# Optimization experiments

Hardware: AMD Instinct MI355X
Metric: run time of the kernel (lower is better)

Reference implementation:

```python
import jax, jax.numpy as jnp
import numpy as np

B, T, C, H = 2, 2048, 1024, 16
D = C // H  # 64
RW, RA, RG = 64, 64, 128  # decay / a / gate LoRA ranks
EPS = 1e-5


def setup_inputs() -> dict:
    key = jax.random.key(0)
    ks = iter(jax.random.split(key, 40))
    n = lambda s, sc=0.02: jax.random.normal(next(ks), s, jnp.float32) * sc
    u = lambda s: jax.random.uniform(next(ks), s, jnp.float32)
    return dict(
        hidden_states=jax.random.normal(next(ks), (B, T, C), jnp.float32),
        # token-mix (time-shift lerp) params
        x_r=u((C,)), x_w=u((C,)), x_k=u((C,)), x_v=u((C,)), x_a=u((C,)), x_g=u((C,)),
        k_k=u((C,)), k_a=u((C,)), r_k=n((H, D), 0.1),
        # square projections (stored [in, out]; x @ W)
        W_r=n((C, C)), W_k=n((C, C)), W_v=n((C, C)), W_o=n((C, C)),
        # LoRA: out = act(x @ A) @ Bm + bias (activation between the two linears)
        w_lora_a=n((C, RW)), w_lora_b=n((RW, C)), w_lora_bias=n((C,), 0.1),
        a_lora_a=n((C, RA)), a_lora_b=n((RA, C)), a_lora_bias=jnp.zeros((C,), jnp.float32),
        g_lora_a=n((C, RG)), g_lora_b=n((RG, C)), g_lora_bias=jnp.zeros((C,), jnp.float32),
        # GroupNorm(num_heads groups over value_dim)
        gn_weight=jnp.ones((C,), jnp.float32), gn_bias=jnp.zeros((C,), jnp.float32),
    )


def _rwkv7_scan(r, log_w, k, v, a, b):
    # all inputs [B, T, H, D]; state S: [B, H, D_v, D_k]
    # S_t = S_{t-1} * diag(exp(log_w_t)) + (S_{t-1} @ a_t) b_t^T + v_t k_t^T
    # o_t = S_t @ r_t
    Bn, Tn, Hn, Dn = r.shape

    def step(S, xs):
        r_t, w_t, k_t, v_t, a_t, b_t = xs  # each [B, H, D]
        sa = jnp.einsum('bhij,bhj->bhi', S, a_t)          # S @ a (pre-decay state)
        S = (S * jnp.exp(w_t)[:, :, None, :]
             + sa[..., None] * b_t[:, :, None, :]
             + v_t[..., None] * k_t[:, :, None, :])
        o_t = jnp.einsum('bhij,bhj->bhi', S, r_t)
        return S, o_t

    S0 = jnp.zeros((Bn, Hn, Dn, Dn), r.dtype)
    xs = tuple(jnp.swapaxes(x, 0, 1) for x in (r, log_w, k, v, a, b))  # [T,B,H,D]
    _, o = jax.lax.scan(step, S0, xs)
    return jnp.swapaxes(o, 0, 1)  # [B, T, H, D]


def reference(hidden_states, x_r, x_w, x_k, x_v, x_a, x_g, k_k, k_a, r_k,
              W_r, W_k, W_v, W_o,
              w_lora_a, w_lora_b, w_lora_bias,
              a_lora_a, a_lora_b, a_lora_bias,
              g_lora_a, g_lora_b, g_lora_bias,
              gn_weight, gn_bias):
    Bn, Tn, Cn = hidden_states.shape
    # time shift: pad one step of zeros at the front, drop last
    shifted = jnp.concatenate([jnp.zeros_like(hidden_states[:, :1]), hidden_states[:, :-1]], axis=1)
    delta = shifted - hidden_states

    xr = hidden_states + delta * x_r
    xw = hidden_states + delta * x_w
    xk = hidden_states + delta * x_k
    xv = hidden_states + delta * x_v
    xa = hidden_states + delta * x_a

    r = xr @ W_r
    log_w = -jax.nn.softplus(-((jnp.tanh(xw @ w_lora_a) @ w_lora_b) + w_lora_bias)) - 0.5
    k = xk @ W_k
    v = xv @ W_v
    a = jax.nn.sigmoid((xa @ a_lora_a) @ a_lora_b + a_lora_bias)
    # g_lora(r): sigmoid activation sits BETWEEN the two LoRA linears
    g = jax.nn.sigmoid(r @ g_lora_a) @ g_lora_b + g_lora_bias

    kk = (k * k_k).reshape(Bn, Tn, H, D)
    kk = kk / jnp.maximum(jnp.linalg.norm(kk, axis=-1, keepdims=True), 1e-12)  # per-head L2 norm
    k = k * (1.0 + (a - 1.0) * k_a)

    rh = r.reshape(Bn, Tn, H, D)
    wh = log_w.reshape(Bn, Tn, H, D)
    kh = k.reshape(Bn, Tn, H, D)
    vh = v.reshape(Bn, Tn, H, D)
    ah = a.reshape(Bn, Tn, H, D)

    o = _rwkv7_scan(rh, wh, kh, vh, -kk, kk * ah)  # [B, T, H, D]

    # GroupNorm over value_dim with H groups (stats per head)
    mu = o.mean(-1, keepdims=True)
    var = ((o - mu) ** 2).mean(-1, keepdims=True)
    o_flat = ((o - mu) * jax.lax.rsqrt(var + EPS)).reshape(Bn, Tn, C) * gn_weight + gn_bias

    bonus = ((rh * kh * r_k).sum(-1, keepdims=True) * vh).reshape(Bn, Tn, C)
    o_flat = o_flat + bonus
    return (o_flat * g) @ W_o
```

## Files before the change

### kernel.cpp

```cpp
#include <hip/hip_runtime.h>
#include <hip/hip_bf16.h>
#include <hip/hip_fp16.h>
#include <stdint.h>
#include <stddef.h>

typedef __hip_bfloat16 bf16;
typedef _Float16 f16;
typedef __attribute__((ext_vector_type(8))) short short8;
typedef __attribute__((ext_vector_type(8))) _Float16 half8;
typedef __attribute__((ext_vector_type(4))) float f32x4;
typedef __attribute__((ext_vector_type(2))) float f32x2;
typedef unsigned short us;

__device__ __forceinline__ float dsigm(float z){ return 1.f/(1.f+expf(-z)); }

template<int CTRL>
__device__ __forceinline__ float dpp_term(float x) {
  int xi = __builtin_bit_cast(int, x);
  int yi = __builtin_amdgcn_update_dpp(0, xi, CTRL, 0xF, 0xF, false);
  return __builtin_bit_cast(float, yi);
}
__device__ __forceinline__ float red8(float x) {
  x += dpp_term<0xB1>(x);
  x += dpp_term<0x4E>(x);
  x += dpp_term<0x141>(x);
  return x;
}

__device__ __forceinline__ void split1(float v, us& h, us& l) {
  bf16 hb = __float2bfloat16(v);
  h = __builtin_bit_cast(us, hb);
  float hf = __bfloat162float(hb);
  bf16 lb = __float2bfloat16(v - hf);
  l = __builtin_bit_cast(us, lb);
}

__device__ __forceinline__ void split8(const float* f, short8& h, short8& l) {
#pragma unroll
  for (int e = 0; e < 8; ++e) {
    us hh, ll;
    split1(f[e], hh, ll);
    h[e] = (short)hh; l[e] = (short)ll;
  }
}

__device__ __forceinline__ void gl16(const f16* g, f16* l) {
  __builtin_amdgcn_global_load_lds((const __attribute__((address_space(1))) void*)g,
                                   (__attribute__((address_space(3))) void*)l, 16, 0, 0);
}

__device__ __forceinline__ void emit16(const float* __restrict__ marr, int c4,
    const float4& cur, const float4& dlt, f16* __restrict__ out, int row)
{
  float4 m = *(const float4*)(marr + c4);
  f16* o = out + (size_t)row*1024 + c4;
  o[0] = (f16)fmaf(dlt.x, m.x, cur.x);
  o[1] = (f16)fmaf(dlt.y, m.y, cur.y);
  o[2] = (f16)fmaf(dlt.z, m.z, cur.z);
  o[3] = (f16)fmaf(dlt.w, m.w, cur.w);
}

__global__ void k_prep(const float* __restrict__ hs,
    const float* __restrict__ mr, const float* __restrict__ mw, const float* __restrict__ mk,
    const float* __restrict__ mv, const float* __restrict__ ma,
    f16* __restrict__ oxr, f16* __restrict__ oxw, f16* __restrict__ oxk,
    f16* __restrict__ oxv, f16* __restrict__ oxa)
{
  int id = blockIdx.x * 256 + threadIdx.x;
  int row = id >> 8;
  int c4 = (id & 255) << 2;
  int t = row & 2047;
  const float* hp = hs + (size_t)row*1024 + c4;
  float4 cur = *(const float4*)hp;
  float4 prev = make_float4(0.f,0.f,0.f,0.f);
  if (t > 0) prev = *(const float4*)(hp - 1024);
  float4 dlt = make_float4(prev.x-cur.x, prev.y-cur.y, prev.z-cur.z, prev.w-cur.w);
  emit16(mr, c4, cur, dlt, oxr, row);
  emit16(mw, c4, cur, dlt, oxw, row);
  emit16(mk, c4, cur, dlt, oxk, row);
  emit16(mv, c4, cur, dlt, oxv, row);
  emit16(ma, c4, cur, dlt, oxa, row);
}

struct SrcP { const float* p[10]; };
struct DstP { f16* p[10]; };

__global__ void k_transpose(SrcP S, DstP Dd)
{
  static constexpr int TR[10]  = {1024,1024,1024,1024,1024,  64,1024,  64,1024, 128};
  static constexpr int TCC[10] = {1024,1024,1024,1024,  64,1024,  64,1024, 128,1024};
  static constexpr int TCP[10] = {1024,1024,1024,1024, 128,1024, 128,1024, 128,1024};
  int z = blockIdx.z;
  int R = TR[z], Cc = TCC[z], Cp = TCP[z];
  int n0 = blockIdx.x * 32, r0 = blockIdx.y * 32;
  if (n0 >= Cp || r0 >= R) return;
  const float* src = S.p[z];
  f16* dst = Dd.p[z];
  int tx = threadIdx.x, ty = threadIdx.y;
  __shared__ float tile[32][33];
  if (n0 < Cc) {
#pragma unroll
    for (int i = 0; i < 4; ++i)
      tile[ty + 8*i][tx] = src[(size_t)(r0 + ty + 8*i)*Cc + n0 + tx];
    __syncthreads();
#pragma unroll
    for (int i = 0; i < 4; ++i)
      dst[(size_t)(n0 + ty + 8*i)*R + r0 + tx] = (f16)tile[tx][ty + 8*i];
  } else {
#pragma unroll
    for (int i = 0; i < 4; ++i)
      dst[(size_t)(n0 + ty + 8*i)*R + r0 + tx] = (f16)0.f;
  }
}

struct GJob {
  const f16* A;
  const f16* Bt;
  float* C;
  f16* Cpk;
  const float* bias;
  int K; int N; int Npk; int ldc; int act;
  int lda; int ldb;
};
struct GJobs { GJob j[5]; };

__global__ __launch_bounds__(256) void k_gemm_fp16(GJobs jobs)
{
  GJob jb = jobs.j[blockIdx.z];
  const int colBase = blockIdx.y * 128;
  if (colBase >= jb.N) return;
  const int rowBase = blockIdx.x * 128;
  __shared__ __align__(16) f16 As[128*32];
  __shared__ __align__(16) f16 Bs[128*32];
  const int tid = threadIdx.x;
  const int l = tid & 63, w = tid >> 6;
  const int wm = w >> 1, wn = w & 1;
  const int lrow = l & 15, kid = (l >> 4) * 8;
  const int nk = jb.K >> 5;

  const int s0 = w*64 + l, s1 = (4 + w)*64 + l;
  const int ar0 = s0 >> 2, ac0 = (s0 & 3) * 8;
  const int ar1 = s1 >> 2, ac1 = (s1 & 3) * 8;
  const int ld0 = w*512, ld1 = (4 + w)*512;
  const f16* Arow0 = jb.A  + (size_t)(rowBase + ar0)*jb.lda + ac0;
  const f16* Arow1 = jb.A  + (size_t)(rowBase + ar1)*jb.lda + ac1;
  const f16* Brow0 = jb.Bt + (size_t)(colBase + ar0)*jb.ldb + ac0;
  const f16* Brow1 = jb.Bt + (size_t)(colBase + ar1)*jb.ldb + ac1;

  f32x4 acc[4][4];
#pragma unroll
  for (int i = 0; i < 4; ++i)
#pragma unroll
    for (int j = 0; j < 4; ++j) { f32x4 z = {0.f,0.f,0.f,0.f}; acc[i][j] = z; }

  for (int kt = 0; kt < nk; ++kt) {
    const int kh = kt*32;
    gl16(Arow0 + kh, &As[ld0]);  gl16(Arow1 + kh, &As[ld1]);
    gl16(Brow0 + kh, &Bs[ld0]);  gl16(Brow1 + kh, &Bs[ld1]);
    __syncthreads();
    half8 ah[4], bh[4];
#pragma unroll
    for (int mt = 0; mt < 4; ++mt) ah[mt] = *(const half8*)&As[(wm*64 + mt*16 + lrow)*32 + kid];
#pragma unroll
    for (int nt = 0; nt < 4; ++nt) bh[nt] = *(const half8*)&Bs[(wn*64 + nt*16 + lrow)*32 + kid];
#pragma unroll
    for (int mt = 0; mt < 4; ++mt)
#pragma unroll
      for (int nt = 0; nt < 4; ++nt)
        acc[mt][nt] = __builtin_amdgcn_mfma_f32_16x16x32_f16(ah[mt], bh[nt], acc[mt][nt], 0, 0, 0);
    __syncthreads();
  }
#pragma unroll
  for (int mt = 0; mt < 4; ++mt) {
    int row = rowBase + wm*64 + mt*16 + (l >> 4)*4;
#pragma unroll
    for (int nt = 0; nt < 4; ++nt) {
      int col = colBase + wn*64 + nt*16 + (l & 15);
      float bv = (jb.bias != nullptr) ? jb.bias[col] : 0.f;
#pragma unroll
      for (int rg = 0; rg < 4; ++rg) {
        float v = acc[mt][nt][rg] + bv;
        if (jb.act == 1)      v = dsigm(v);
        else if (jb.act == 2) v = tanhf(v);
        else if (jb.act == 3) v = 0.60653066f * dsigm(v);
        if (jb.C) jb.C[(size_t)(row + rg)*jb.ldc + col] = v;
        if (jb.Cpk && col < jb.Npk)
          jb.Cpk[(size_t)(row + rg)*jb.Npk + col] = (f16)v;
      }
    }
  }
}

__global__ void k_scanprep(f16* __restrict__ kA, f16* __restrict__ aA,
                           const float* __restrict__ kkw, const float* __restrict__ kaw,
                           f16* __restrict__ kkA)
{
  int idx = blockIdx.x * 256 + threadIdx.x;
  size_t gt8 = (size_t)idx * 8;
  int ch = (int)(gt8 & 1023);
  half8 k8 = *(const half8*)(kA + gt8);
  half8 a8 = *(const half8*)(aA + gt8);
  float kw[8], ka_[8];
  *(float4*)&kw[0]  = *(const float4*)(kkw + ch);
  *(float4*)&kw[4]  = *(const float4*)(kkw + ch + 4);
  *(float4*)&ka_[0] = *(const float4*)(kaw + ch);
  *(float4*)&ka_[4] = *(const float4*)(kaw + ch + 4);
  float kkv[8]; float ss = 0.f;
#pragma unroll
  for (int e = 0; e < 8; ++e) { kkv[e] = (float)k8[e] * kw[e]; ss += kkv[e]*kkv[e]; }
  ss += __shfl_xor(ss, 1); ss += __shfl_xor(ss, 2); ss += __shfl_xor(ss, 4);
  float inv = 1.f / fmaxf(sqrtf(ss), 1e-12f);
  half8 kkn8, bb8, kup8;
#pragma unroll
  for (int e = 0; e < 8; ++e) {
    float kkn = kkv[e] * inv;
    float av = (float)a8[e];
    kkn8[e] = (f16)kkn;
    bb8[e]  = (f16)(kkn * av);
    kup8[e] = (f16)((float)k8[e] * fmaf(av - 1.f, ka_[e], 1.f));
  }
  *(half8*)(kkA + gt8) = kkn8;
  *(half8*)(aA + gt8)  = bb8;
  *(half8*)(kA + gt8)  = kup8;
}

__device__ __forceinline__ void step_pk(const float* __restrict__ sb, int s,
    f32x2* u2, f32x2* p2, float* __restrict__ o0A, float* __restrict__ zA,
    size_t base, int i, int q, int j0)
{
  f32x2 ew2[4], kk2[4], bb2[4], kv2[4], rr2[4];
#pragma unroll
  for (int hh = 0; hh < 2; ++hh) {
    float4 a0 = *(const float4*)(sb + 0    + s*64 + j0 + hh*4);
    float4 a1 = *(const float4*)(sb + 512  + s*64 + j0 + hh*4);
    float4 a2 = *(const float4*)(sb + 1024 + s*64 + j0 + hh*4);
    float4 a3 = *(const float4*)(sb + 1536 + s*64 + j0 + hh*4);
    float4 a4 = *(const float4*)(sb + 2048 + s*64 + j0 + hh*4);
    ew2[hh*2+0] = f32x2{a0.x, a0.y}; ew2[hh*2+1] = f32x2{a0.z, a0.w};
    kk2[hh*2+0] = f32x2{a1.x, a1.y}; kk2[hh*2+1] = f32x2{a1.z, a1.w};
    bb2[hh*2+0] = f32x2{a2.x, a2.y}; bb2[hh*2+1] = f32x2{a2.z, a2.w};
    kv2[hh*2+0] = f32x2{a3.x, a3.y}; kv2[hh*2+1] = f32x2{a3.z, a3.w};
    rr2[hh*2+0] = f32x2{a4.x, a4.y}; rr2[hh*2+1] = f32x2{a4.z, a4.w};
  }
  float vi = sb[2560 + s*64 + i];

  f32x2 uk2 = u2[0]*kk2[0], pk2 = p2[0]*kk2[0];
#pragma unroll
  for (int e = 1; e < 4; ++e) { uk2 += u2[e]*kk2[e]; pk2 += p2[e]*kk2[e]; }
  float uk = red8(uk2.x + uk2.y);
  float pk = red8(pk2.x + pk2.y);
  const f32x2 su2 = {-uk, -uk}, sp2 = {-pk, -pk}, vi2 = {vi, vi};
  f32x2 oo2 = {0.f, 0.f}, zz2 = {0.f, 0.f};
#pragma unroll
  for (int e = 0; e < 4; ++e) {
    f32x2 uu = u2[e]*ew2[e] + su2*bb2[e] + vi2*kv2[e];
    u2[e] = uu; oo2 += uu*rr2[e];
    f32x2 pp = p2[e]*ew2[e] + sp2*bb2[e];
    p2[e] = pp; zz2 += pp*rr2[e];
  }
  float oo = red8(oo2.x + oo2.y);
  float zz = red8(zz2.x + zz2.y);
  if (q == 0) { o0A[base + i] = oo; zA[base + i] = zz; }
}

__global__ __launch_bounds__(512) void k_scan_p1(
    const f16* __restrict__ rA, const f16* __restrict__ ewA,
    const f16* __restrict__ kA, const f16* __restrict__ vA,
    const f16* __restrict__ kkA, const f16* __restrict__ bbA,
    float* __restrict__ o0A, float* __restrict__ zA,
    float* __restrict__ UcA, float* __restrict__ PTcA)
{
  const int blk = blockIdx.x;
  const int bh = blk & 31, c = blk >> 5;
  const int b = bh >> 4, h = bh & 15;
  const int tid = threadIdx.x;
  const int i = tid >> 3, q = tid & 7, j0 = q * 8;
  const size_t base0 = (size_t)b*2048*1024 + (size_t)h*64 + (size_t)(c*64)*1024;

  __shared__ __align__(16) float smem[6144];

  const int active = (tid < 384);
  const int a0 = tid >> 6, rm0 = tid & 63, s0 = rm0 >> 3, f0 = rm0 & 7;
  const f16* pa0 = (a0==0) ? ewA : (a0==1) ? kkA : (a0==2) ? bbA :
                   (a0==3) ? kA  : (a0==4) ? rA  : vA;
  const f16* src0 = pa0 + base0 + (size_t)s0*1024 + f0*8;
  const int dst0 = a0*512 + s0*64 + f0*8;

  f32x2 u2[4], p2[4];
#pragma unroll
  for (int e = 0; e < 4; ++e) {
    u2[e] = f32x2{0.f, 0.f};
    float p0 = (j0 + 2*e     == i) ? 1.f : 0.f;
    float p1 = (j0 + 2*e + 1 == i) ? 1.f : 0.f;
    p2[e] = f32x2{p0, p1};
  }

  if (active) {
    half8 hh = *(const half8*)(src0);
    float4 lo = {(float)hh[0], (float)hh[1], (float)hh[2], (float)hh[3]};
    float4 hi = {(float)hh[4], (float)hh[5], (float)hh[6], (float)hh[7]};
    *(float4*)&smem[dst0]     = lo;
    *(float4*)&smem[dst0 + 4] = hi;
  }
  __syncthreads();

  int curb = 0;
  for (int g = 0; g < 8; ++g) {
    half8 n0;
    if (g < 7 && active) n0 = *(const half8*)(src0 + (size_t)(g+1)*8192);
    const float* sb = smem + curb*3072;
#pragma unroll
    for (int s = 0; s < 8; ++s)
      step_pk(sb, s, u2, p2, o0A, zA, base0 + (size_t)(g*8 + s)*1024, i, q, j0);
    if (g < 7 && active) {
      float4 lo = {(float)n0[0], (float)n0[1], (float)n0[2], (float)n0[3]};
      float4 hi = {(float)n0[4], (float)n0[5], (float)n0[6], (float)n0[7]};
      *(float4*)&smem[(curb^1)*3072 + dst0]     = lo;
      *(float4*)&smem[(curb^1)*3072 + dst0 + 4] = hi;
    }
    __syncthreads();
    curb ^= 1;
  }

  const size_t cbase = ((size_t)(bh*32 + c)) * 4096;
  *(float4*)(UcA + cbase + (size_t)i*64 + j0)     = make_float4(u2[0].x,u2[0].y,u2[1].x,u2[1].y);
  *(float4*)(UcA + cbase + (size_t)i*64 + j0 + 4) = make_float4(u2[2].x,u2[2].y,u2[3].x,u2[3].y);
  float (*lds)[65] = (float(*)[65])smem;
#pragma unroll
  for (int e = 0; e < 4; ++e) {
    lds[i][j0 + 2*e]     = p2[e].x;
    lds[i][j0 + 2*e + 1] = p2[e].y;
  }
  __syncthreads();
  float4 w0 = make_float4(lds[j0+0][i], lds[j0+1][i], lds[j0+2][i], lds[j0+3][i]);
  float4 w1 = make_float4(lds[j0+4][i], lds[j0+5][i], lds[j0+6][i], lds[j0+7][i]);
  *(float4*)(PTcA + cbase + (size_t)i*64 + j0)     = w0;
  *(float4*)(PTcA + cbase + (size_t)i*64 + j0 + 4) = w1;
}

__device__ __forceinline__ void chain_body(int c, int bh, int w, int lr, int lq,
    float (&Slds)[64][65], f32x4 (&acc)[4],
    float (&u_c)[4][4], float4 (&p_c)[2][2],
    float (&u_n)[4][4], float4 (&p_n)[2][2],
    const float* __restrict__ UcA, const float* __restrict__ PTcA,
    float* __restrict__ S0A)
{
  const size_t s0base = ((size_t)bh*32 + c) * 4096;
#pragma unroll
  for (int mt = 0; mt < 4; ++mt)
#pragma unroll
    for (int rg = 0; rg < 4; ++rg) {
      Slds[mt*16 + lq*4 + rg][w*16 + lr] = acc[mt][rg];
      if (c > 0) S0A[s0base + (size_t)(mt*16 + lq*4 + rg)*64 + w*16 + lr] = acc[mt][rg];
    }
  __syncthreads();
  if (c + 1 < 32) {
    const size_t nbase = ((size_t)bh*32 + c + 1) * 4096;
#pragma unroll
    for (int mt = 0; mt < 4; ++mt)
#pragma unroll
      for (int rg = 0; rg < 4; ++rg)
        u_n[mt][rg] = UcA[nbase + (size_t)(mt*16 + lq*4 + rg)*64 + w*16 + lr];
#pragma unroll
    for (int kt = 0; kt < 2; ++kt)
#pragma unroll
      for (int hh = 0; hh < 2; ++hh)
        p_n[kt][hh] = *(const float4*)(PTcA + nbase + (size_t)(w*16 + lr)*64 + kt*32 + lq*8 + hh*4);
  }
  short8 pbh[2], pbl[2];
#pragma unroll
  for (int kt = 0; kt < 2; ++kt) {
    float f[8] = {p_c[kt][0].x, p_c[kt][0].y, p_c[kt][0].z, p_c[kt][0].w,
                  p_c[kt][1].x, p_c[kt][1].y, p_c[kt][1].z, p_c[kt][1].w};
    split8(f, pbh[kt], pbl[kt]);
  }
  f32x4 nacc[4];
#pragma unroll
  for (int mt = 0; mt < 4; ++mt) {
    f32x4 z = {u_c[mt][0], u_c[mt][1], u_c[mt][2], u_c[mt][3]};
    nacc[mt] = z;
  }
#pragma unroll
  for (int kt = 0; kt < 2; ++kt)
#pragma unroll
    for (int mt = 0; mt < 4; ++mt) {
      float f[8];
#pragma unroll
      for (int e = 0; e < 8; ++e) f[e] = Slds[mt*16 + lr][kt*32 + lq*8 + e];
      short8 sah, sal;
      split8(f, sah, sal);
      nacc[mt] = __builtin_amdgcn_mfma_f32_16x16x32_bf16(sah, pbh[kt], nacc[mt], 0, 0, 0);
      nacc[mt] = __builtin_amdgcn_mfma_f32_16x16x32_bf16(sal, pbh[kt], nacc[mt], 0, 0, 0);
      nacc[mt] = __builtin_amdgcn_mfma_f32_16x16x32_bf16(sah, pbl[kt], nacc[mt], 0, 0, 0);
    }
#pragma unroll
  for (int mt = 0; mt < 4; ++mt) acc[mt] = nacc[mt];
  __syncthreads();
}

__global__ __launch_bounds__(256) void k_chain(
    const float* __restrict__ UcA, const float* __restrict__ PTcA,
    float* __restrict__ S0A)
{
  const int bh = blockIdx.x;
  const int l = threadIdx.x & 63, w = threadIdx.x >> 6;
  const int lr = l & 15, lq = l >> 4;
  __shared__ float Slds[64][65];

  f32x4 acc[4];
#pragma unroll
  for (int mt = 0; mt < 4; ++mt) { f32x4 z = {0.f,0.f,0.f,0.f}; acc[mt] = z; }

  float u0[4][4], u1[4][4];
  float4 p0[2][2], p1[2][2];
  {
    const size_t cbase = (size_t)bh * 32 * 4096;
#pragma unroll
    for (int mt = 0; mt < 4; ++mt)
#pragma unroll
      for (int rg = 0; rg < 4; ++rg)
        u0[mt][rg] = UcA[cbase + (size_t)(mt*16 + lq*4 + rg)*64 + w*16 + lr];
#pragma unroll
    for (int kt = 0; kt < 2; ++kt)
#pragma unroll
      for (int hh = 0; hh < 2; ++hh)
        p0[kt][hh] = *(const float4*)(PTcA + cbase + (size_t)(w*16 + lr)*64 + kt*32 + lq*8 + hh*4);
  }
  for (int c = 0; c < 32; c += 2) {
    chain_body(c,     bh, w, lr, lq, Slds, acc, u0, p0, u1, p1, UcA, PTcA, S0A);
    chain_body(c + 1, bh, w, lr, lq, Slds, acc, u1, p1, u0, p0, UcA, PTcA, S0A);
  }
}

__global__ __launch_bounds__(256) void k_corrpost(
    const float* __restrict__ S0A, const float* __restrict__ zA,
    const float* __restrict__ o0A, const f16* __restrict__ rA,
    const f16* __restrict__ kA, const f16* __restrict__ vA,
    const float* __restrict__ rk, const float* __restrict__ gnw,
    const float* __restrict__ gnb, const f16* __restrict__ gA,
    f16* __restrict__ yH)
{
  const int blk = blockIdx.x;
  const int bh = blk & 31;
  const int c  = blk >> 5;
  const int b = bh >> 4, h = bh & 15;
  const int l = threadIdx.x & 63, w = threadIdx.x >> 6;
  const int lr = l & 15, lq = l >> 4;

  f32x4 a2[4];
#pragma unroll
  for (int nt = 0; nt < 4; ++nt) { f32x4 z = {0.f,0.f,0.f,0.f}; a2[nt] = z; }

  if (c > 0) {
    const size_t s0base = ((size_t)bh*32 + c) * 4096;
    short8 sbh[4][2], sbl[4][2];
#pragma unroll
    for (int nt = 0; nt < 4; ++nt)
#pragma unroll
      for (int kt = 0; kt < 2; ++kt) {
        float f[8];
#pragma unroll
        for (int e = 0; e < 8; ++e)
          f[e] = S0A[s0base + (size_t)(nt*16 + lr)*64 + kt*32 + lq*8 + e];
        split8(f, sbh[nt][kt], sbl[nt][kt]);
      }
    short8 zh[2], zl[2];
#pragma unroll
    for (int kt = 0; kt < 2; ++kt) {
      const float* zp = zA + ((size_t)(b*2048 + c*64 + w*16 + lr)*16 + h)*64 + kt*32 + lq*8;
      float f[8];
#pragma unroll
      for (int e = 0; e < 8; ++e) f[e] = zp[e];
      split8(f, zh[kt], zl[kt]);
    }
#pragma unroll
    for (int kt = 0; kt < 2; ++kt)
#pragma unroll
      for (int nt = 0; nt < 4; ++nt) {
        a2[nt] = __builtin_amdgcn_mfma_f32_16x16x32_bf16(zh[kt], sbh[nt][kt], a2[nt], 0, 0, 0);
        a2[nt] = __builtin_amdgcn_mfma_f32_16x16x32_bf16(zl[kt], sbh[nt][kt], a2[nt], 0, 0, 0);
        a2[nt] = __builtin_amdgcn_mfma_f32_16x16x32_bf16(zh[kt], sbl[nt][kt], a2[nt], 0, 0, 0);
      }
  }

#pragma unroll
  for (int rg = 0; rg < 4; ++rg) {
    const int tl = w*16 + lq*4 + rg;
    const size_t trow = (size_t)(b*2048 + c*64 + tl);
    const size_t rb = trow*1024 + h*64;
    float o4[4], v4[4];
    float sum = 0.f, pr = 0.f;
#pragma unroll
    for (int nt = 0; nt < 4; ++nt) {
      const int ii = nt*16 + lr;
      float o = o0A[rb + ii] + a2[nt][rg];
      o4[nt] = o; sum += o;
      v4[nt] = (float)vA[rb + ii];
      pr += (float)rA[rb + ii] * (float)kA[rb + ii] * rk[h*64 + ii];
    }
    sum += __shfl_xor(sum,1); sum += __shfl_xor(sum,2);
    sum += __shfl_xor(sum,4); sum += __shfl_xor(sum,8);
    pr  += __shfl_xor(pr,1);  pr  += __shfl_xor(pr,2);
    pr  += __shfl_xor(pr,4);  pr  += __shfl_xor(pr,8);
    float mean = sum * (1.f/64.f);
    float vp = 0.f;
#pragma unroll
    for (int nt = 0; nt < 4; ++nt) { float d = o4[nt]-mean; vp += d*d; }
    vp += __shfl_xor(vp,1); vp += __shfl_xor(vp,2);
    vp += __shfl_xor(vp,4); vp += __shfl_xor(vp,8);
    float inv = rsqrtf(vp*(1.f/64.f) + 1e-5f);
#pragma unroll
    for (int nt = 0; nt < 4; ++nt) {
      const int ii = nt*16 + lr;
      const int ch = h*64 + ii;
      float y = (o4[nt]-mean)*inv*gnw[ch] + gnb[ch];
      y = fmaf(pr, v4[nt], y);
      y *= (float)gA[rb + ii];
      yH[trow*1024 + ch] = (f16)y;
    }
  }
}

extern "C" void kernel_launch(void* const* d_in, const int* in_sizes, int n_in,
                              void* d_out, int out_size, void* d_ws, size_t ws_size,
                              hipStream_t stream)
{
  (void)in_sizes; (void)n_in; (void)out_size; (void)ws_size;
  const float* hs     = (const float*)d_in[0];
  const float* x_r    = (const float*)d_in[1];
  const float* x_w    = (const float*)d_in[2];
  const float* x_k    = (const float*)d_in[3];
  const float* x_v    = (const float*)d_in[4];
  const float* x_a    = (const float*)d_in[5];
  const float* k_k    = (const float*)d_in[7];
  const float* k_a    = (const float*)d_in[8];
  const float* r_k    = (const float*)d_in[9];
  const float* W_r    = (const float*)d_in[10];
  const float* W_k    = (const float*)d_in[11];
  const float* W_v    = (const float*)d_in[12];
  const float* W_o    = (const float*)d_in[13];
  const float* wla    = (const float*)d_in[14];
  const float* wlb    = (const float*)d_in[15];
  const float* wlbias = (const float*)d_in[16];
  const float* ala    = (const float*)d_in[17];
  const float* alb    = (const float*)d_in[18];
  const float* albias = (const float*)d_in[19];
  const float* gla    = (const float*)d_in[20];
  const float* glb    = (const float*)d_in[21];
  const float* glbias = (const float*)d_in[22];
  const float* gnw    = (const float*)d_in[23];
  const float* gnb    = (const float*)d_in[24];

  char* ws = (char*)d_ws;
  size_t cur = 0;
  auto take = [&](size_t bytes) { size_t o = cur; cur += (bytes + 255) & ~(size_t)255; return o; };

  f16* xr_h = (f16*)(ws + take((size_t)4096*1024*2));
  f16* xw_h = (f16*)(ws + take((size_t)4096*1024*2));
  f16* xk_h = (f16*)(ws + take((size_t)4096*1024*2));
  f16* xv_h = (f16*)(ws + take((size_t)4096*1024*2));
  f16* xa_h = (f16*)(ws + take((size_t)4096*1024*2));
  f16* Wr_p  = (f16*)(ws + take((size_t)1024*1024*2));
  f16* Wk_p  = (f16*)(ws + take((size_t)1024*1024*2));
  f16* Wv_p  = (f16*)(ws + take((size_t)1024*1024*2));
  f16* Wo_p  = (f16*)(ws + take((size_t)1024*1024*2));
  f16* wla_p = (f16*)(ws + take((size_t)128*1024*2));
  f16* wlb_p = (f16*)(ws + take((size_t)1024*64*2));
  f16* ala_p = (f16*)(ws + take((size_t)128*1024*2));
  f16* alb_p = (f16*)(ws + take((size_t)1024*64*2));
  f16* gla_p = (f16*)(ws + take((size_t)128*1024*2));
  f16* glb_p = (f16*)(ws + take((size_t)1024*128*2));
  f16* r_h  = (f16*)(ws + take((size_t)4096*1024*2));
  f16* k_h  = (f16*)(ws + take((size_t)4096*1024*2));
  f16* v_h  = (f16*)(ws + take((size_t)4096*1024*2));
  f16* kk_h = (f16*)(ws + take((size_t)4096*1024*2));
  f16* g_h  = (f16*)(ws + take((size_t)4096*1024*2));
  f16* t2w  = (f16*)(ws + take((size_t)4096*64*2));
  f16* t2a  = (f16*)(ws + take((size_t)4096*64*2));
  f16* t2g  = (f16*)(ws + take((size_t)4096*128*2));
  float* z_f  = (float*)(ws + take((size_t)4096*1024*4));
  float* Uc_f = (float*)(ws + take((size_t)4096*1024*4));
  float* PT_f = (float*)(ws + take((size_t)4096*1024*4));
  f16*   ew_h = xw_h;
  f16*   a_h  = xa_h;
  f16*   y_h  = xr_h;
  float* S0_f = (float*)xk_h;
  float* oF   = (float*)d_out;

  k_prep<<<4096, 256, 0, stream>>>(hs, x_r, x_w, x_k, x_v, x_a,
                                   xr_h, xw_h, xk_h, xv_h, xa_h);
  SrcP sp; DstP dp;
  sp.p[0]=W_r; sp.p[1]=W_k; sp.p[2]=W_v; sp.p[3]=W_o;
  sp.p[4]=wla; sp.p[5]=wlb; sp.p[6]=ala; sp.p[7]=alb; sp.p[8]=gla; sp.p[9]=glb;
  dp.p[0]=Wr_p; dp.p[1]=Wk_p; dp.p[2]=Wv_p; dp.p[3]=Wo_p;
  dp.p[4]=wla_p; dp.p[5]=wlb_p; dp.p[6]=ala_p; dp.p[7]=alb_p; dp.p[8]=gla_p; dp.p[9]=glb_p;
  k_transpose<<<dim3(32,32,10), dim3(32,8), 0, stream>>>(sp, dp);

  GJobs J{};
  auto job = [](const f16* A, const f16* Bt, float* C, f16* Cpk, const float* bias,
                int K, int N, int Npk, int ldc, int act, int lda, int ldb) {
    GJob j; j.A=A; j.Bt=Bt; j.C=C; j.Cpk=Cpk; j.bias=bias;
    j.K=K; j.N=N; j.Npk=Npk; j.ldc=ldc; j.act=act; j.lda=lda; j.ldb=ldb;
    return j;
  };

  J.j[0] = job(xr_h, Wr_p,  nullptr, r_h, nullptr, 1024, 1024, 1024, 0, 0, 1024, 1024);
  J.j[1] = job(xk_h, Wk_p,  nullptr, k_h, nullptr, 1024, 1024, 1024, 0, 0, 1024, 1024);
  J.j[2] = job(xv_h, Wv_p,  nullptr, v_h, nullptr, 1024, 1024, 1024, 0, 0, 1024, 1024);
  J.j[3] = job(xw_h, wla_p, nullptr, t2w, nullptr, 1024, 128,  64,   0, 2, 1024, 1024);
  J.j[4] = job(xa_h, ala_p, nullptr, t2a, nullptr, 1024, 128,  64,   0, 0, 1024, 1024);
  k_gemm_fp16<<<dim3(32,8,5), 256, 0, stream>>>(J);

  J = GJobs{};
  J.j[0] = job(t2w, wlb_p, nullptr, ew_h, wlbias, 64,   1024, 1024, 0, 3, 64,   64);
  J.j[1] = job(t2a, alb_p, nullptr, a_h,  albias, 64,   1024, 1024, 0, 1, 64,   64);
  J.j[2] = job(r_h, gla_p, nullptr, t2g,  nullptr, 1024, 128,  128,  0, 1, 1024, 1024);
  k_gemm_fp16<<<dim3(32,8,3), 256, 0, stream>>>(J);

  J = GJobs{};
  J.j[0] = job(t2g, glb_p, nullptr, g_h, glbias, 128, 1024, 1024, 0, 0, 128, 128);
  k_gemm_fp16<<<dim3(32,8,1), 256, 0, stream>>>(J);

  k_scanprep<<<2048, 256, 0, stream>>>(k_h, a_h, k_k, k_a, kk_h);

  k_scan_p1<<<1024, 512, 0, stream>>>(r_h, ew_h, k_h, v_h, kk_h, a_h, oF, z_f, Uc_f, PT_f);
  k_chain<<<32, 256, 0, stream>>>(Uc_f, PT_f, S0_f);

  k_corrpost<<<1024, 256, 0, stream>>>(S0_f, z_f, oF, r_h, k_h, v_h,
                                       r_k, gnw, gnb, g_h, y_h);

  J = GJobs{};
  J.j[0] = job(y_h, Wo_p, (float*)d_out, nullptr, nullptr, 1024, 1024, 0, 1024, 0, 1024, 1024);
  k_gemm_fp16<<<dim3(32,8,1), 256, 0, stream>>>(J);
}
```

Baseline: 331.8 us.

## Double GEMM K-tile to 64 and XOR-swizzle LDS layout

The fp16 MFMA GEMM now stages a 64-wide K slice per iteration instead of 32, which halves the number of barrier pairs per tile. The shared-memory rows are also stored with an XOR swizzle of 16-byte units keyed on the row index, so that fragment reads avoid bank conflicts. This doubles LDS use to 32 KB per block, which can lower occupancy, and it requires K to be a multiple of 64.

```diff
diff --git a/kernel.cpp b/kernel.cpp
--- a/kernel.cpp
+++ b/kernel.cpp
@@ -130,22 +130,25 @@
   const int colBase = blockIdx.y * 128;
   if (colBase >= jb.N) return;
   const int rowBase = blockIdx.x * 128;
-  __shared__ __align__(16) f16 As[128*32];
-  __shared__ __align__(16) f16 Bs[128*32];
+  __shared__ __align__(16) f16 As[128*64];
+  __shared__ __align__(16) f16 Bs[128*64];
   const int tid = threadIdx.x;
   const int l = tid & 63, w = tid >> 6;
   const int wm = w >> 1, wn = w & 1;
-  const int lrow = l & 15, kid = (l >> 4) * 8;
-  const int nk = jb.K >> 5;
-
-  const int s0 = w*64 + l, s1 = (4 + w)*64 + l;
-  const int ar0 = s0 >> 2, ac0 = (s0 & 3) * 8;
-  const int ar1 = s1 >> 2, ac1 = (s1 & 3) * 8;
-  const int ld0 = w*512, ld1 = (4 + w)*512;
-  const f16* Arow0 = jb.A  + (size_t)(rowBase + ar0)*jb.lda + ac0;
-  const f16* Arow1 = jb.A  + (size_t)(rowBase + ar1)*jb.lda + ac1;
-  const f16* Brow0 = jb.Bt + (size_t)(colBase + ar0)*jb.ldb + ac0;
-  const f16* Brow1 = jb.Bt + (size_t)(colBase + ar1)*jb.ldb + ac1;
+  const int lrow = l & 15;
+  const int nk = jb.K >> 6;
+
+  const f16* Arow[4]; const f16* Brow[4]; int ld[4];
+#pragma unroll
+  for (int i2 = 0; i2 < 4; ++i2) {
+    int s = (i2*4 + w)*64 + l;
+    int ar = s >> 3;
+    int unit = s & 7;
+    int acs = (unit ^ (ar & 7)) * 8;
+    Arow[i2] = jb.A  + (size_t)(rowBase + ar)*jb.lda + acs;
+    Brow[i2] = jb.Bt + (size_t)(colBase + ar)*jb.ldb + acs;
+    ld[i2] = (i2*4 + w) * 512;
+  }
 
   f32x4 acc[4][4];
 #pragma unroll
@@ -154,20 +157,34 @@
     for (int j = 0; j < 4; ++j) { f32x4 z = {0.f,0.f,0.f,0.f}; acc[i][j] = z; }
 
   for (int kt = 0; kt < nk; ++kt) {
-    const int kh = kt*32;
-    gl16(Arow0 + kh, &As[ld0]);  gl16(Arow1 + kh, &As[ld1]);
-    gl16(Brow0 + kh, &Bs[ld0]);  gl16(Brow1 + kh, &Bs[ld1]);
+    const int kh = kt*64;
+#pragma unroll
+    for (int i2 = 0; i2 < 4; ++i2) {
+      gl16(Arow[i2] + kh, &As[ld[i2]]);
+      gl16(Brow[i2] + kh, &Bs[ld[i2]]);
+    }
     __syncthreads();
-    half8 ah[4], bh[4];
-#pragma unroll
-    for (int mt = 0; mt < 4; ++mt) ah[mt] = *(const half8*)&As[(wm*64 + mt*16 + lrow)*32 + kid];
-#pragma unroll
-    for (int nt = 0; nt < 4; ++nt) bh[nt] = *(const half8*)&Bs[(wn*64 + nt*16 + lrow)*32 + kid];
-#pragma unroll
-    for (int mt = 0; mt < 4; ++mt)
-#pragma unroll
-      for (int nt = 0; nt < 4; ++nt)
-        acc[mt][nt] = __builtin_amdgcn_mfma_f32_16x16x32_f16(ah[mt], bh[nt], acc[mt][nt], 0, 0, 0);
+#pragma unroll
+    for (int ks = 0; ks < 2; ++ks) {
+      half8 ah[4], bh[4];
+#pragma unroll
+      for (int mt = 0; mt < 4; ++mt) {
+        int row = wm*64 + mt*16 + lrow;
+        int cu = ks*4 + (l >> 4);
+        ah[mt] = *(const half8*)&As[row*64 + ((cu ^ (row & 7)) * 8)];
+      }
+#pragma unroll
+      for (int nt = 0; nt < 4; ++nt) {
+        int row = wn*64 + nt*16 + lrow;
+        int cu = ks*4 + (l >> 4);
+        bh[nt] = *(const half8*)&Bs[row*64 + ((cu ^ (row & 7)) * 8)];
+      }
+#pragma unroll
+      for (int mt = 0; mt < 4; ++mt)
+#pragma unroll
+        for (int nt = 0; nt < 4; ++nt)
+          acc[mt][nt] = __builtin_amdgcn_mfma_f32_16x16x32_f16(ah[mt], bh[nt], acc[mt][nt], 0, 0, 0);
+    }
     __syncthreads();
   }
 #pragma unroll
```

Result: faster. 322.8 us (-2.7%).
